# Performance work log

Hardware: AMD Instinct MI355X
Metric: run time of the kernel (lower is better)

## Reference

```python
import jax, jax.numpy as jnp
import numpy as np

N_NODES = 50000
N_EDGES = 800000
IN_FEATS = 64
HID_FEATS = 64


def setup_inputs() -> dict:
    key = jax.random.key(0)
    ks = jax.random.split(key, 5)
    x = jax.random.normal(ks[0], (N_NODES, IN_FEATS), dtype=jnp.float32)
    src = jax.random.randint(ks[1], (N_EDGES,), 0, N_NODES)
    dst = jax.random.randint(ks[2], (N_EDGES,), 0, N_NODES)
    # GraphConv parameters (Glorot-ish init, bias zeros as in dgl defaults)
    W1 = jax.random.normal(ks[3], (IN_FEATS, HID_FEATS), dtype=jnp.float32) / np.sqrt(IN_FEATS)
    b1 = jnp.zeros((HID_FEATS,), dtype=jnp.float32)
    W2 = jax.random.normal(ks[4], (HID_FEATS, IN_FEATS), dtype=jnp.float32) / np.sqrt(HID_FEATS)
    b2 = jnp.zeros((IN_FEATS,), dtype=jnp.float32)
    return {"x": x, "src": src, "dst": dst, "W1": W1, "b1": b1, "W2": W2, "b2": b2}


def _graph_conv(x, src, dst, W, b, n_nodes):
    """dgl GraphConv with norm='both': D_dst^{-1/2} A D_src^{-1/2} X W + b."""
    ones = jnp.ones((src.shape[0],), dtype=x.dtype)
    deg_out = jax.ops.segment_sum(ones, src, num_segments=n_nodes)
    deg_in = jax.ops.segment_sum(ones, dst, num_segments=n_nodes)
    norm_out = jnp.where(deg_out > 0, jax.lax.rsqrt(jnp.maximum(deg_out, 1.0)), 0.0)
    norm_in = jnp.where(deg_in > 0, jax.lax.rsqrt(jnp.maximum(deg_in, 1.0)), 0.0)
    h = x * norm_out[:, None]                                  # [N, F] scaled by src norm
    agg = jax.ops.segment_sum(h[src], dst, num_segments=n_nodes)  # gather over edges + scatter-add
    return (agg * norm_in[:, None]) @ W + b


def reference(x, src, dst, W1, b1, W2, b2):
    n, d = x.shape
    # dHdx: conv -> tanh -> conv
    y = jnp.tanh(_graph_conv(x, src, dst, W1, b1, n))
    y = _graph_conv(y, src, dst, W2, b2, n)
    # J = cat([I[d//2:], -I[:d//2]])  -> symplectic [[0, I], [-I, 0]]
    I = jnp.eye(d, dtype=x.dtype)
    J = jnp.concatenate([I[d // 2:], -I[: d // 2]], axis=0)
    # get_D is undefined in the source module; treated as zero dissipation term.
    return y @ J.T
```

## Files before the change

### kernel.cpp

```cpp
#include <hip/hip_runtime.h>
#include <hip/hip_bf16.h>
#include <math.h>

#define N_NODES 50000
#define N_EDGES 800000
#define F 64
#define NPAD 50048
#define NBLK ((N_NODES + 255) / 256)

#define P_HIST 256
#define CHUNK (N_EDGES / P_HIST)
#define WORDS8 12500
#define RBLK8 ((WORDS8 + 255) / 256)

#define TW 20
#define RV3BLK (WORDS8 / TW)
#define TS 260

#define LROW 36
#define LBLK ((N_NODES + 31) / 32)

typedef short short8 __attribute__((ext_vector_type(8)));
typedef float f32x4 __attribute__((ext_vector_type(4)));

__device__ inline unsigned short f2bf(float f) {
    unsigned u = __float_as_uint(f);
    unsigned r = (u + 0x7fffu + ((u >> 16) & 1u)) >> 16;
    return (unsigned short)r;
}
__device__ inline float bf2f(unsigned v) { return __uint_as_float(v << 16); }
__device__ inline float bf2f_hi(unsigned v) { return __uint_as_float(v & 0xffff0000u); }

__device__ inline unsigned wave_incl_scan(unsigned v, int lane) {
    #pragma unroll
    for (int d = 1; d < 64; d <<= 1) {
        unsigned u = __shfl_up(v, d, 64);
        if (lane >= d) v += u;
    }
    return v;
}


__global__ __launch_bounds__(256) void hist_kernel(
    const int* __restrict__ src, const int* __restrict__ dst,
    unsigned* __restrict__ histd, unsigned* __restrict__ hists)
{
    __shared__ unsigned lds[WORDS8];
    int p = blockIdx.x, t = threadIdx.x;
    int e0 = p * CHUNK;
    for (int hp = 0; hp < 2; ++hp) {
        const int* col = hp ? src : dst;
        unsigned* outp = (hp ? hists : histd) + (size_t)p * WORDS8;
        for (int i = t; i < WORDS8; i += 256) lds[i] = 0;
        __syncthreads();
        for (int i = t; i < CHUNK; i += 256) {
            int v = col[e0 + i];
            atomicAdd(&lds[v >> 2], 1u << ((v & 3) * 8));
        }
        __syncthreads();
        for (int i = t; i < WORDS8; i += 256) outp[i] = lds[i];
        __syncthreads();
    }
}

__global__ __launch_bounds__(256) void reduce_v3_kernel(
    unsigned* __restrict__ histd, const unsigned* __restrict__ hists,
    float* __restrict__ norm_in, float* __restrict__ norm_out,
    int* __restrict__ row_off, unsigned* __restrict__ wordsum)
{
    __shared__ unsigned lds[TW * TS];
    int t = threadIdx.x, b = blockIdx.x;
    int lane = t & 63, ww = t >> 6;
    int w0 = b * TW;

    {
        uint4* gp = (uint4*)(histd + (size_t)t * WORDS8 + w0);
        #pragma unroll
        for (int i = 0; i < TW / 4; ++i) {
            uint4 v = gp[i];
            lds[(i * 4 + 0) * TS + t] = v.x;
            lds[(i * 4 + 1) * TS + t] = v.y;
            lds[(i * 4 + 2) * TS + t] = v.z;
            lds[(i * 4 + 3) * TS + t] = v.w;
        }
    }
    __syncthreads();
    #pragma unroll
    for (int k = 0; k < TW / 4; ++k) {
        int lw = ww + k * 4;
        uint4 h = *(uint4*)(lds + lw * TS + 4 * lane);
        unsigned lsum = h.x + h.y + h.z + h.w;
        unsigned inc = lsum;
        #pragma unroll
        for (int d = 1; d < 64; d <<= 1) {
            unsigned u = __shfl_up(inc, d, 64);
            if (lane >= d) inc += u;
        }
        unsigned run = inc - lsum;
        uint4 o;
        o.x = run; run += h.x;
        o.y = run; run += h.y;
        o.z = run; run += h.z;
        o.w = run;
        *(uint4*)(lds + lw * TS + 4 * lane) = o;
        unsigned total = __shfl(inc, 63, 64);
        if (lane == 0) {
            int w = w0 + lw;
            unsigned d0 = total & 255u, d1 = (total >> 8) & 255u;
            unsigned d2 = (total >> 16) & 255u, d3 = total >> 24;
            norm_in[4 * w]     = d0 ? rsqrtf((float)d0) : 0.f;
            norm_in[4 * w + 1] = d1 ? rsqrtf((float)d1) : 0.f;
            norm_in[4 * w + 2] = d2 ? rsqrtf((float)d2) : 0.f;
            norm_in[4 * w + 3] = d3 ? rsqrtf((float)d3) : 0.f;
            int4 r;
            r.x = 0; r.y = (int)d0; r.z = (int)(d0 + d1); r.w = (int)(d0 + d1 + d2);
            *(int4*)(row_off + 4 * w) = r;
            wordsum[w] = d0 + d1 + d2 + d3;
        }
    }
    __syncthreads();
    {
        uint4* gp = (uint4*)(histd + (size_t)t * WORDS8 + w0);
        #pragma unroll
        for (int i = 0; i < TW / 4; ++i) {
            uint4 v;
            v.x = lds[(i * 4 + 0) * TS + t];
            v.y = lds[(i * 4 + 1) * TS + t];
            v.z = lds[(i * 4 + 2) * TS + t];
            v.w = lds[(i * 4 + 3) * TS + t];
            gp[i] = v;
        }
    }
    __syncthreads();

    {
        const uint4* gp = (const uint4*)(hists + (size_t)t * WORDS8 + w0);
        #pragma unroll
        for (int i = 0; i < TW / 4; ++i) {
            uint4 v = gp[i];
            lds[(i * 4 + 0) * TS + t] = v.x;
            lds[(i * 4 + 1) * TS + t] = v.y;
            lds[(i * 4 + 2) * TS + t] = v.z;
            lds[(i * 4 + 3) * TS + t] = v.w;
        }
    }
    __syncthreads();
    #pragma unroll
    for (int k = 0; k < TW / 4; ++k) {
        int lw = ww + k * 4;
        uint4 h = *(uint4*)(lds + lw * TS + 4 * lane);
        unsigned s = h.x + h.y + h.z + h.w;
        #pragma unroll
        for (int d = 1; d < 64; d <<= 1) s += __shfl_xor(s, d, 64);
        if (lane == 0) {
            int w = w0 + lw;
            unsigned t0 = s & 255u, t1 = (s >> 8) & 255u;
            unsigned t2 = (s >> 16) & 255u, t3 = s >> 24;
            norm_out[4 * w]     = t0 ? rsqrtf((float)t0) : 0.f;
            norm_out[4 * w + 1] = t1 ? rsqrtf((float)t1) : 0.f;
            norm_out[4 * w + 2] = t2 ? rsqrtf((float)t2) : 0.f;
            norm_out[4 * w + 3] = t3 ? rsqrtf((float)t3) : 0.f;
        }
    }
}

__global__ __launch_bounds__(256) void scanw_kernel(
    const unsigned* __restrict__ wordsum, int* __restrict__ row_off,
    unsigned* __restrict__ blockSums)
{
    __shared__ unsigned wsum[4];
    int t = threadIdx.x, b = blockIdx.x;
    int w = b * 256 + t;
    unsigned v = (w < WORDS8) ? wordsum[w] : 0u;
    int lane = t & 63, wid = t >> 6;
    unsigned inc = wave_incl_scan(v, lane);
    if (lane == 63) wsum[wid] = inc;
    __syncthreads();
    if (t == 0) {
        unsigned acc = 0;
        #pragma unroll
        for (int q = 0; q < 4; ++q) { unsigned x = wsum[q]; wsum[q] = acc; acc += x; }
    }
    __syncthreads();
    unsigned excl = inc - v + wsum[wid];
    if (w < WORDS8) {
        int4 r = *(int4*)(row_off + 4 * w);
        r.x += (int)excl; r.y += (int)excl; r.z += (int)excl; r.w += (int)excl;
        *(int4*)(row_off + 4 * w) = r;
    }
    if (t == 255) blockSums[b] = excl + v;
}

__global__ __launch_bounds__(256) void scan_fin_kernel(
    const unsigned* __restrict__ blockSums, int* __restrict__ row_off)
{
    __shared__ unsigned off_s;
    int t = threadIdx.x, b = blockIdx.x;
    if (t < 64) {
        unsigned v = (t < b) ? blockSums[t] : 0u;
        #pragma unroll
        for (int d = 1; d < 64; d <<= 1) v += __shfl_xor(v, d, 64);
        if (t == 0) off_s = v;
    }
    __syncthreads();
    int off = (int)off_s;
    int w = b * 256 + t;
    if (w < WORDS8) {
        int4 r = *(int4*)(row_off + 4 * w);
        r.x += off; r.y += off; r.z += off; r.w += off;
        *(int4*)(row_off + 4 * w) = r;
    }
    if (w == 0) row_off[N_NODES] = N_EDGES;
}

__global__ __launch_bounds__(256) void scatter_kernel(
    const int* __restrict__ src, const int* __restrict__ dst,
    const int* __restrict__ row_off, const unsigned* __restrict__ histd,
    int* __restrict__ csr_src)
{
    __shared__ unsigned lds[WORDS8];
    int p = blockIdx.x, t = threadIdx.x;
    int e0 = p * CHUNK;
    const unsigned* pref = histd + (size_t)p * WORDS8;
    for (int i = t; i < WORDS8; i += 256) lds[i] = 0;
    __syncthreads();
    for (int i = t; i < CHUNK; i += 256) {
        int d = dst[e0 + i];
        int sh = (d & 3) * 8;
        unsigned old = atomicAdd(&lds[d >> 2], 1u << sh);
        unsigned rank = (old >> sh) & 255u;
        unsigned pre  = (pref[d >> 2] >> sh) & 255u;
        csr_src[row_off[d] + (int)(pre + rank)] = src[e0 + i];
    }
}


__global__ __launch_bounds__(256) void degrees_kernel(
    const int* __restrict__ src, const int* __restrict__ dst,
    unsigned* __restrict__ deg_out_u, unsigned* __restrict__ deg_in_u)
{
    int e = blockIdx.x * 256 + threadIdx.x;
    if (e < N_EDGES) {
        atomicAdd(&deg_out_u[src[e]], 1u);
        atomicAdd(&deg_in_u[dst[e]], 1u);
    }
}

__global__ __launch_bounds__(256) void fb_scan_a_kernel(
    const unsigned* __restrict__ deg_in_u, const unsigned* __restrict__ deg_out_u,
    float* __restrict__ norm_out, float* __restrict__ norm_in,
    int* __restrict__ row_off, unsigned* __restrict__ blockSums)
{
    __shared__ unsigned wsum[4];
    int t = threadIdx.x, b = blockIdx.x;
    int idx = b * 256 + t;
    unsigned v = 0, dout = 0;
    if (idx < N_NODES) { v = deg_in_u[idx]; dout = deg_out_u[idx]; }
    int lane = t & 63, wid = t >> 6;
    unsigned inc = wave_incl_scan(v, lane);
    if (lane == 63) wsum[wid] = inc;
    __syncthreads();
    if (t == 0) {
        unsigned acc = 0;
        #pragma unroll
        for (int q = 0; q < 4; ++q) { unsigned x = wsum[q]; wsum[q] = acc; acc += x; }
    }
    __syncthreads();
    unsigned excl = inc - v + wsum[wid];
    if (idx < N_NODES) {
        row_off[idx] = (int)excl;
        norm_in[idx]  = v    ? rsqrtf((float)v)    : 0.f;
        norm_out[idx] = dout ? rsqrtf((float)dout) : 0.f;
    }
    if (t == 255) blockSums[b] = excl + v;
}

__global__ __launch_bounds__(256) void fb_scan_b_kernel(
    const unsigned* __restrict__ blockSums, unsigned* __restrict__ blockOff, int cnt)
{
    __shared__ unsigned wsum[4];
    int t = threadIdx.x;
    unsigned v = (t < cnt) ? blockSums[t] : 0u;
    int lane = t & 63, wid = t >> 6;
    unsigned inc = wave_incl_scan(v, lane);
    if (lane == 63) wsum[wid] = inc;
    __syncthreads();
    if (t == 0) {
        unsigned acc = 0;
        #pragma unroll
        for (int q = 0; q < 4; ++q) { unsigned x = wsum[q]; wsum[q] = acc; acc += x; }
    }
    __syncthreads();
    if (t < cnt) blockOff[t] = inc - v + wsum[wid];
}

__global__ __launch_bounds__(256) void fb_scan_c_kernel(
    const unsigned* __restrict__ blockOff, int* __restrict__ row_off,
    unsigned* __restrict__ cursor)
{
    int idx = blockIdx.x * 256 + threadIdx.x;
    if (idx < N_NODES) {
        int v = row_off[idx] + (int)blockOff[blockIdx.x];
        row_off[idx] = v;
        cursor[idx] = (unsigned)v;
    }
    if (idx == 0) row_off[N_NODES] = N_EDGES;
}

__global__ __launch_bounds__(256) void fb_csr_fill_kernel(
    const int* __restrict__ src, const int* __restrict__ dst,
    unsigned* __restrict__ cursor, int* __restrict__ csr_src)
{
    int e = blockIdx.x * 256 + threadIdx.x;
    if (e < N_EDGES) {
        unsigned p = atomicAdd(&cursor[dst[e]], 1u);
        csr_src[p] = src[e];
    }
}


__global__ __launch_bounds__(256) void prescale_kernel(
    const float* __restrict__ x, const float* __restrict__ norm_out,
    unsigned* __restrict__ xb)
{
    int t = blockIdx.x * 256 + threadIdx.x;
    if (t < N_NODES * 32) {
        int n = t >> 5;
        float w = norm_out[n];
        float2 v = ((const float2*)x)[t];
        xb[t] = (unsigned)f2bf(v.x * w) | ((unsigned)f2bf(v.y * w) << 16);
    }
}

__device__ inline void block_agg32(
    const unsigned* __restrict__ tab, const float* __restrict__ norm_in,
    const int* __restrict__ row_off, const int* __restrict__ csr_src,
    int nb, unsigned* lds)
{
    int tid = threadIdx.x;
    int wid = tid >> 6, lane = tid & 63;
    int g = lane >> 3, lp = lane & 7;
    int m = wid * 8 + g;
    int n = nb + m;
    float a0 = 0.f, a1 = 0.f, a2 = 0.f, a3 = 0.f;
    float a4 = 0.f, a5 = 0.f, a6 = 0.f, a7 = 0.f;
    float w = 0.f;
    if (n < N_NODES) {
        int beg = row_off[n];
        int end = row_off[n + 1];
        w = norm_in[n];
        int e = beg;
        for (; e + 3 < end; e += 4) {
            int s0 = csr_src[e], s1 = csr_src[e + 1];
            int s2 = csr_src[e + 2], s3 = csr_src[e + 3];
            uint4 v0 = *(const uint4*)(tab + (size_t)s0 * 32 + lp * 4);
            uint4 v1 = *(const uint4*)(tab + (size_t)s1 * 32 + lp * 4);
            uint4 v2 = *(const uint4*)(tab + (size_t)s2 * 32 + lp * 4);
            uint4 v3 = *(const uint4*)(tab + (size_t)s3 * 32 + lp * 4);
            a0 += bf2f(v0.x & 0xffffu); a1 += bf2f_hi(v0.x);
            a2 += bf2f(v0.y & 0xffffu); a3 += bf2f_hi(v0.y);
            a4 += bf2f(v0.z & 0xffffu); a5 += bf2f_hi(v0.z);
            a6 += bf2f(v0.w & 0xffffu); a7 += bf2f_hi(v0.w);
            a0 += bf2f(v1.x & 0xffffu); a1 += bf2f_hi(v1.x);
            a2 += bf2f(v1.y & 0xffffu); a3 += bf2f_hi(v1.y);
            a4 += bf2f(v1.z & 0xffffu); a5 += bf2f_hi(v1.z);
            a6 += bf2f(v1.w & 0xffffu); a7 += bf2f_hi(v1.w);
            a0 += bf2f(v2.x & 0xffffu); a1 += bf2f_hi(v2.x);
            a2 += bf2f(v2.y & 0xffffu); a3 += bf2f_hi(v2.y);
            a4 += bf2f(v2.z & 0xffffu); a5 += bf2f_hi(v2.z);
            a6 += bf2f(v2.w & 0xffffu); a7 += bf2f_hi(v2.w);
            a0 += bf2f(v3.x & 0xffffu); a1 += bf2f_hi(v3.x);
            a2 += bf2f(v3.y & 0xffffu); a3 += bf2f_hi(v3.y);
            a4 += bf2f(v3.z & 0xffffu); a5 += bf2f_hi(v3.z);
            a6 += bf2f(v3.w & 0xffffu); a7 += bf2f_hi(v3.w);
        }
        for (; e < end; ++e) {
            int s0 = csr_src[e];
            uint4 v0 = *(const uint4*)(tab + (size_t)s0 * 32 + lp * 4);
            a0 += bf2f(v0.x & 0xffffu); a1 += bf2f_hi(v0.x);
            a2 += bf2f(v0.y & 0xffffu); a3 += bf2f_hi(v0.y);
            a4 += bf2f(v0.z & 0xffffu); a5 += bf2f_hi(v0.z);
            a6 += bf2f(v0.w & 0xffffu); a7 += bf2f_hi(v0.w);
        }
    }
    uint4 o;
    o.x = (unsigned)f2bf(a0 * w) | ((unsigned)f2bf(a1 * w) << 16);
    o.y = (unsigned)f2bf(a2 * w) | ((unsigned)f2bf(a3 * w) << 16);
    o.z = (unsigned)f2bf(a4 * w) | ((unsigned)f2bf(a5 * w) << 16);
    o.w = (unsigned)f2bf(a6 * w) | ((unsigned)f2bf(a7 * w) << 16);
    *(uint4*)(lds + m * LROW + lp * 4) = o;
}

__global__ __launch_bounds__(256) void layer1_fused_kernel(
    const unsigned* __restrict__ tab, const float* __restrict__ norm_in,
    const float* __restrict__ norm_out, const int* __restrict__ row_off,
    const int* __restrict__ csr_src, const float* __restrict__ Wm,
    const float* __restrict__ bias, unsigned short* __restrict__ hb)
{
    __shared__ unsigned lds[32 * LROW];
    int tid = threadIdx.x;
    int wid = tid >> 6, lane = tid & 63;
    int q = lane >> 4, lp16 = lane & 15;
    int nb = blockIdx.x * 32;

    short8 bfrag[2];
    #pragma unroll
    for (int kt = 0; kt < 2; ++kt)
        #pragma unroll
        for (int j = 0; j < 8; ++j)
            bfrag[kt][j] = (short)f2bf(Wm[(kt * 32 + q * 8 + j) * F + wid * 16 + lp16]);

    block_agg32(tab, norm_in, row_off, csr_src, nb, lds);
    __syncthreads();

    int nn = wid * 16 + lp16;
    float bv = bias[nn];
    #pragma unroll
    for (int rg = 0; rg < 2; ++rg) {
        short8 afrag[2];
        #pragma unroll
        for (int kt = 0; kt < 2; ++kt)
            afrag[kt] = *(const short8*)(lds + (rg * 16 + lp16) * LROW + kt * 16 + q * 4);
        f32x4 acc = (f32x4){0.f, 0.f, 0.f, 0.f};
        #pragma unroll
        for (int kt = 0; kt < 2; ++kt)
            acc = __builtin_amdgcn_mfma_f32_16x16x32_bf16(afrag[kt], bfrag[kt], acc, 0, 0, 0);
        #pragma unroll
        for (int r = 0; r < 4; ++r) {
            int row = nb + rg * 16 + q * 4 + r;
            if (row < N_NODES) {
                float z = tanhf(acc[r] + bv) * norm_out[row];
                hb[(size_t)row * F + nn] = f2bf(z);
            }
        }
    }
}

__global__ __launch_bounds__(256) void layer2_fused_kernel(
    const unsigned* __restrict__ tab, const float* __restrict__ norm_in,
    const int* __restrict__ row_off, const int* __restrict__ csr_src,
    const float* __restrict__ Wm, const float* __restrict__ bias,
    float* __restrict__ out)
{
    __shared__ unsigned lds[32 * LROW];
    int tid = threadIdx.x;
    int wid = tid >> 6, lane = tid & 63;
    int q = lane >> 4, lp16 = lane & 15;
    int nb = blockIdx.x * 32;

    short8 bfrag[2];
    #pragma unroll
    for (int kt = 0; kt < 2; ++kt)
        #pragma unroll
        for (int j = 0; j < 8; ++j)
            bfrag[kt][j] = (short)f2bf(Wm[(kt * 32 + q * 8 + j) * F + wid * 16 + lp16]);

    block_agg32(tab, norm_in, row_off, csr_src, nb, lds);
    __syncthreads();

    int nn = wid * 16 + lp16;
    float bv = bias[nn];
    int oc = (nn + 32) & 63;
    float sgn = (nn < 32) ? -1.f : 1.f;
    #pragma unroll
    for (int rg = 0; rg < 2; ++rg) {
        short8 afrag[2];
        #pragma unroll
        for (int kt = 0; kt < 2; ++kt)
            afrag[kt] = *(const short8*)(lds + (rg * 16 + lp16) * LROW + kt * 16 + q * 4);
        f32x4 acc = (f32x4){0.f, 0.f, 0.f, 0.f};
        #pragma unroll
        for (int kt = 0; kt < 2; ++kt)
            acc = __builtin_amdgcn_mfma_f32_16x16x32_bf16(afrag[kt], bfrag[kt], acc, 0, 0, 0);
        #pragma unroll
        for (int r = 0; r < 4; ++r) {
            int row = nb + rg * 16 + q * 4 + r;
            if (row < N_NODES) {
                float z = acc[r] + bv;
                out[(size_t)row * F + oc] = sgn * z;
            }
        }
    }
}

extern "C" void kernel_launch(void* const* d_in, const int* in_sizes, int n_in,
                              void* d_out, int out_size, void* d_ws, size_t ws_size,
                              hipStream_t stream) {
    const float* x   = (const float*)d_in[0];
    const int*   src = (const int*)d_in[1];
    const int*   dst = (const int*)d_in[2];
    const float* W1  = (const float*)d_in[3];
    const float* b1  = (const float*)d_in[4];
    const float* W2  = (const float*)d_in[5];
    const float* b2  = (const float*)d_in[6];
    float* out = (float*)d_out;

    unsigned* ws = (unsigned*)d_ws;
    float*    norm_out = (float*)ws;
    float*    norm_in  = (float*)(ws + NPAD);
    int*      row_off  = (int*)(ws + 2 * NPAD);
    int*      csr_src  = (int*)(ws + 3 * NPAD);
    unsigned* xb       = ws + 3 * NPAD + N_EDGES;
    unsigned* hbu      = xb + (size_t)NPAD * 32;
    unsigned* blockSums= hbu + (size_t)NPAD * 32;
    unsigned* blockOff = blockSums + 256;
    unsigned* wordsum  = blockOff + 256;
    unsigned* tail     = wordsum + WORDS8;
    unsigned* histd = tail;
    unsigned* hists = histd + (size_t)P_HIST * WORDS8;
    size_t need_new = ((size_t)(tail - ws) + 2 * (size_t)P_HIST * WORDS8) * 4;

    if (ws_size >= need_new) {
        hist_kernel<<<P_HIST, 256, 0, stream>>>(src, dst, histd, hists);
        reduce_v3_kernel<<<RV3BLK, 256, 0, stream>>>(histd, hists, norm_in, norm_out, row_off, wordsum);
        scanw_kernel<<<RBLK8, 256, 0, stream>>>(wordsum, row_off, blockSums);
        scan_fin_kernel<<<RBLK8, 256, 0, stream>>>(blockSums, row_off);
        scatter_kernel<<<P_HIST, 256, 0, stream>>>(src, dst, row_off, histd, csr_src);
    } else {
        unsigned* deg_out_u = tail;
        unsigned* deg_in_u  = tail + NPAD;
        unsigned* cursor    = tail + 2 * NPAD;
        hipMemsetAsync(deg_out_u, 0, 2 * NPAD * sizeof(unsigned), stream);
        degrees_kernel<<<(N_EDGES + 255) / 256, 256, 0, stream>>>(src, dst, deg_out_u, deg_in_u);
        fb_scan_a_kernel<<<NBLK, 256, 0, stream>>>(deg_in_u, deg_out_u, norm_out, norm_in, row_off, blockSums);
        fb_scan_b_kernel<<<1, 256, 0, stream>>>(blockSums, blockOff, NBLK);
        fb_scan_c_kernel<<<NBLK, 256, 0, stream>>>(blockOff, row_off, cursor);
        fb_csr_fill_kernel<<<(N_EDGES + 255) / 256, 256, 0, stream>>>(src, dst, cursor, csr_src);
    }

    prescale_kernel<<<(N_NODES * 32 + 255) / 256, 256, 0, stream>>>(x, norm_out, xb);
    layer1_fused_kernel<<<LBLK, 256, 0, stream>>>(
        xb, norm_in, norm_out, row_off, csr_src, W1, b1, (unsigned short*)hbu);

    layer2_fused_kernel<<<LBLK, 256, 0, stream>>>(
        hbu, norm_in, row_off, csr_src, W2, b2, out);
}
```

Measured before the change: 168.5 us.

## Split histogram and scatter kernels across node-range slices for more blocks

The per-chunk histogram and CSR scatter kernels are split into four blocks per edge chunk, each owning a quarter of the node-word range. Each block now keeps a smaller LDS histogram, which lets more blocks stay resident, and the histogram kernel counts src and dst in a single pass. The scatter kernel also preloads its prefix slice into LDS. In exchange every block reads the full edge chunk, so edge index reads from global memory are repeated four times.

```diff
diff --git a/kernel.cpp b/kernel.cpp
--- a/kernel.cpp
+++ b/kernel.cpp
@@ -12,6 +12,9 @@
 #define CHUNK (N_EDGES / P_HIST)
 #define WORDS8 12500
 #define RBLK8 ((WORDS8 + 255) / 256)
+#define RSPLIT 4
+#define WR (WORDS8 / RSPLIT)
+#define HBLK (P_HIST * RSPLIT)
 
 #define TW 20
 #define RV3BLK (WORDS8 / TW)
@@ -41,26 +44,30 @@
 }
 
 
-__global__ __launch_bounds__(256) void hist_kernel(
+__global__ __launch_bounds__(256) void hist2_kernel(
     const int* __restrict__ src, const int* __restrict__ dst,
     unsigned* __restrict__ histd, unsigned* __restrict__ hists)
 {
-    __shared__ unsigned lds[WORDS8];
-    int p = blockIdx.x, t = threadIdx.x;
+    __shared__ unsigned ldd[WR];
+    __shared__ unsigned lsd[WR];
+    int bid = blockIdx.x, t = threadIdx.x;
+    int p = bid >> 2, r = bid & 3;
     int e0 = p * CHUNK;
-    for (int hp = 0; hp < 2; ++hp) {
-        const int* col = hp ? src : dst;
-        unsigned* outp = (hp ? hists : histd) + (size_t)p * WORDS8;
-        for (int i = t; i < WORDS8; i += 256) lds[i] = 0;
-        __syncthreads();
-        for (int i = t; i < CHUNK; i += 256) {
-            int v = col[e0 + i];
-            atomicAdd(&lds[v >> 2], 1u << ((v & 3) * 8));
-        }
-        __syncthreads();
-        for (int i = t; i < WORDS8; i += 256) outp[i] = lds[i];
-        __syncthreads();
-    }
+    unsigned wbase = (unsigned)(r * WR);
+    for (int i = t; i < WR; i += 256) { ldd[i] = 0; lsd[i] = 0; }
+    __syncthreads();
+    for (int i = t; i < CHUNK; i += 256) {
+        int d = dst[e0 + i];
+        int s = src[e0 + i];
+        unsigned wd = ((unsigned)d >> 2) - wbase;
+        unsigned ws = ((unsigned)s >> 2) - wbase;
+        if (wd < WR) atomicAdd(&ldd[wd], 1u << ((d & 3) * 8));
+        if (ws < WR) atomicAdd(&lsd[ws], 1u << ((s & 3) * 8));
+    }
+    __syncthreads();
+    unsigned* outd = histd + (size_t)p * WORDS8 + r * WR;
+    unsigned* outs = hists + (size_t)p * WORDS8 + r * WR;
+    for (int i = t; i < WR; i += 256) { outd[i] = ldd[i]; outs[i] = lsd[i]; }
 }
 
 __global__ __launch_bounds__(256) void reduce_v3_kernel(
@@ -213,24 +220,31 @@
     if (w == 0) row_off[N_NODES] = N_EDGES;
 }
 
-__global__ __launch_bounds__(256) void scatter_kernel(
+__global__ __launch_bounds__(256) void scatter2_kernel(
     const int* __restrict__ src, const int* __restrict__ dst,
     const int* __restrict__ row_off, const unsigned* __restrict__ histd,
     int* __restrict__ csr_src)
 {
-    __shared__ unsigned lds[WORDS8];
-    int p = blockIdx.x, t = threadIdx.x;
+    __shared__ unsigned rk[WR];
+    __shared__ unsigned pf[WR];
+    int bid = blockIdx.x, t = threadIdx.x;
+    int p = bid >> 2, r = bid & 3;
     int e0 = p * CHUNK;
-    const unsigned* pref = histd + (size_t)p * WORDS8;
-    for (int i = t; i < WORDS8; i += 256) lds[i] = 0;
+    unsigned wbase = (unsigned)(r * WR);
+    const unsigned* pref = histd + (size_t)p * WORDS8 + r * WR;
+    for (int i = t; i < WR; i += 256) { rk[i] = 0; pf[i] = pref[i]; }
     __syncthreads();
     for (int i = t; i < CHUNK; i += 256) {
         int d = dst[e0 + i];
-        int sh = (d & 3) * 8;
-        unsigned old = atomicAdd(&lds[d >> 2], 1u << sh);
-        unsigned rank = (old >> sh) & 255u;
-        unsigned pre  = (pref[d >> 2] >> sh) & 255u;
-        csr_src[row_off[d] + (int)(pre + rank)] = src[e0 + i];
+        int s = src[e0 + i];
+        unsigned wd = ((unsigned)d >> 2) - wbase;
+        if (wd < WR) {
+            int sh = (d & 3) * 8;
+            unsigned old = atomicAdd(&rk[wd], 1u << sh);
+            unsigned rank = (old >> sh) & 255u;
+            unsigned pre  = (pf[wd] >> sh) & 255u;
+            csr_src[row_off[d] + (int)(pre + rank)] = s;
+        }
     }
 }
 
@@ -511,11 +525,11 @@
     size_t need_new = ((size_t)(tail - ws) + 2 * (size_t)P_HIST * WORDS8) * 4;
 
     if (ws_size >= need_new) {
-        hist_kernel<<<P_HIST, 256, 0, stream>>>(src, dst, histd, hists);
+        hist2_kernel<<<HBLK, 256, 0, stream>>>(src, dst, histd, hists);
         reduce_v3_kernel<<<RV3BLK, 256, 0, stream>>>(histd, hists, norm_in, norm_out, row_off, wordsum);
         scanw_kernel<<<RBLK8, 256, 0, stream>>>(wordsum, row_off, blockSums);
         scan_fin_kernel<<<RBLK8, 256, 0, stream>>>(blockSums, row_off);
-        scatter_kernel<<<P_HIST, 256, 0, stream>>>(src, dst, row_off, histd, csr_src);
+        scatter2_kernel<<<HBLK, 256, 0, stream>>>(src, dst, row_off, histd, csr_src);
     } else {
         unsigned* deg_out_u = tail;
         unsigned* deg_in_u  = tail + NPAD;
```

Result: no change. 165.2 us (-1.9%).
